# Kernel optimization log

Hardware: AMD Instinct MI355X
Metric: run time of the kernel (lower is better)

## Reference

```python
import jax, jax.numpy as jnp
import numpy as np

VOCAB = 50257
H = 1024
T = 4096


def setup_inputs() -> dict:
    key = jax.random.key(0)
    ks = jax.random.split(key, 6)
    scale = 1.0 / np.sqrt(H)  # matches torch LSTM uniform(-1/sqrt(H), 1/sqrt(H)) scale
    return {
        "tokens": jax.random.randint(ks[0], (T,), 0, VOCAB),
        "emb": jax.random.normal(ks[1], (VOCAB, H), dtype=jnp.float32) * 0.02,
        "w_ih": jax.random.uniform(ks[2], (4 * H, H), jnp.float32, -scale, scale),
        "w_hh": jax.random.uniform(ks[3], (4 * H, H), jnp.float32, -scale, scale),
        "b_ih": jax.random.uniform(ks[4], (4 * H,), jnp.float32, -scale, scale),
        "b_hh": jax.random.uniform(ks[5], (4 * H,), jnp.float32, -scale, scale),
    }


def _lstm(x, w_ih, w_hh, b_ih, b_hh):
    # x: [T, H]. Precompute input-side gate projections for all timesteps.
    gx = x @ w_ih.T + (b_ih + b_hh)  # [T, 4H]

    def step(carry, g_t):
        h, c = carry  # [H], [H]
        gates = g_t + h @ w_hh.T  # [4H]
        i, f, g, o = jnp.split(gates, 4)  # torch gate order: input, forget, cell, output
        i = jax.nn.sigmoid(i)
        f = jax.nn.sigmoid(f)
        g = jnp.tanh(g)
        o = jax.nn.sigmoid(o)
        c = f * c + i * g
        h = o * jnp.tanh(c)
        return (h, c), h

    h0 = jnp.zeros((H,), x.dtype)
    c0 = jnp.zeros((H,), x.dtype)
    (h_f, c_f), hs = jax.lax.scan(step, (h0, c0), gx)
    return hs, h_f, c_f  # hs: [T, H]


def reference(tokens, emb, w_ih, w_hh, b_ih, b_hh):
    x = emb[tokens]  # [T, H] embedding lookup
    hs, h_f, c_f = _lstm(x, w_ih, w_hh, b_ih, b_hh)
    output = hs[None, :, :]          # [1, T, H]  (batch_first, batch=1)
    h_n = h_f[None, None, :]         # [1, 1, H]
    c_n = c_f[None, None, :]         # [1, 1, H]
    return (output, (h_n, c_n))
```

## Files before the change

### kernel.cpp

```cpp
#include <hip/hip_runtime.h>
#include <hip/hip_bf16.h>

#define HD   1024
#define GD   4096
#define TT   4096
#define NWG  256
#define MBS  16

#define BM 128
#define BN 128
#define BK 16
#define LDP 132

__global__ __launch_bounds__(256, 2) void gemm_gx(
    const int* __restrict__ tokens,
    const float* __restrict__ emb,
    const float* __restrict__ Wih,
    const float* __restrict__ bih,
    const float* __restrict__ bhh,
    float* __restrict__ gxout)
{
    __shared__ float As[BK][LDP];
    __shared__ float Bs[BK][LDP];
    const int tid = threadIdx.x;
    const int m0 = blockIdx.x * BM;
    const int n0 = blockIdx.y * BN;
    const int tx = tid & 15;
    const int ty = tid >> 4;

    const int quad = tid & 3;
    const int r0   = tid >> 2;
    const int tok0 = tokens[m0 + r0];
    const int tok1 = tokens[m0 + r0 + 64];

    float acc[8][8] = {};

    for (int kt = 0; kt < HD; kt += BK) {
        float4 av0 = *reinterpret_cast<const float4*>(
            &emb[(size_t)tok0 * HD + kt + quad * 4]);
        float4 bv0 = *reinterpret_cast<const float4*>(
            &Wih[(size_t)(n0 + r0) * HD + kt + quad * 4]);
        float4 av1 = *reinterpret_cast<const float4*>(
            &emb[(size_t)tok1 * HD + kt + quad * 4]);
        float4 bv1 = *reinterpret_cast<const float4*>(
            &Wih[(size_t)(n0 + r0 + 64) * HD + kt + quad * 4]);
        As[quad * 4 + 0][r0] = av0.x;
        As[quad * 4 + 1][r0] = av0.y;
        As[quad * 4 + 2][r0] = av0.z;
        As[quad * 4 + 3][r0] = av0.w;
        Bs[quad * 4 + 0][r0] = bv0.x;
        Bs[quad * 4 + 1][r0] = bv0.y;
        Bs[quad * 4 + 2][r0] = bv0.z;
        Bs[quad * 4 + 3][r0] = bv0.w;
        As[quad * 4 + 0][r0 + 64] = av1.x;
        As[quad * 4 + 1][r0 + 64] = av1.y;
        As[quad * 4 + 2][r0 + 64] = av1.z;
        As[quad * 4 + 3][r0 + 64] = av1.w;
        Bs[quad * 4 + 0][r0 + 64] = bv1.x;
        Bs[quad * 4 + 1][r0 + 64] = bv1.y;
        Bs[quad * 4 + 2][r0 + 64] = bv1.z;
        Bs[quad * 4 + 3][r0 + 64] = bv1.w;
        __syncthreads();
#pragma unroll
        for (int k = 0; k < BK; ++k) {
            float4 a0 = *reinterpret_cast<const float4*>(&As[k][ty * 8]);
            float4 a1 = *reinterpret_cast<const float4*>(&As[k][ty * 8 + 4]);
            float4 b0 = *reinterpret_cast<const float4*>(&Bs[k][tx * 8]);
            float4 b1 = *reinterpret_cast<const float4*>(&Bs[k][tx * 8 + 4]);
            float a[8] = {a0.x, a0.y, a0.z, a0.w, a1.x, a1.y, a1.z, a1.w};
            float b[8] = {b0.x, b0.y, b0.z, b0.w, b1.x, b1.y, b1.z, b1.w};
#pragma unroll
            for (int i = 0; i < 8; ++i)
#pragma unroll
                for (int j = 0; j < 8; ++j)
                    acc[i][j] += a[i] * b[j];
        }
        __syncthreads();
    }

    float bias[8];
#pragma unroll
    for (int j = 0; j < 8; ++j) {
        int n = n0 + tx * 8 + j;
        bias[j] = bih[n] + bhh[n];
    }
#pragma unroll
    for (int i = 0; i < 8; ++i) {
        size_t o = (size_t)(m0 + ty * 8 + i) * GD + n0 + tx * 8;
        float4 s0 = {acc[i][0] + bias[0], acc[i][1] + bias[1],
                     acc[i][2] + bias[2], acc[i][3] + bias[3]};
        float4 s1 = {acc[i][4] + bias[4], acc[i][5] + bias[5],
                     acc[i][6] + bias[6], acc[i][7] + bias[7]};
        *reinterpret_cast<float4*>(&gxout[o]) = s0;
        *reinterpret_cast<float4*>(&gxout[o + 4]) = s1;
    }
}

__device__ __forceinline__ float sigmoid_(float x) {
    return 1.f / (1.f + __expf(-x));
}
__device__ __forceinline__ float tanh_(float x) {
    return __builtin_fmaf(2.f, 1.f / (1.f + __expf(-2.f * x)), -1.f);
}
__device__ __forceinline__ float bcast_(float v, int l) {
    return __uint_as_float(__builtin_amdgcn_readlane(__float_as_uint(v), l));
}
__device__ __forceinline__ void lds_barrier_() {
    asm volatile("s_waitcnt lgkmcnt(0)" ::: "memory");
    __builtin_amdgcn_s_barrier();
}

__global__ __launch_bounds__(256, 1) void lstm_scan(
    const float* __restrict__ gx,
    const float* __restrict__ whh,
    float* __restrict__ out,
    unsigned long long* __restrict__ hbuf)
{
    const int tid   = threadIdx.x;
    const int b     = blockIdx.x;
    const int lane  = tid & 63;
    const int wv    = tid >> 6;
    const int chunk = lane & 15;
    const int gate  = lane >> 4;
    const int j     = b * 4 + wv;
    const int R     = gate * HD + j;

    float w[64];
    {
        const float* wrow = whh + (size_t)R * HD;
#pragma unroll
        for (int q = 0; q < 16; ++q) {
            float4 v = *reinterpret_cast<const float4*>(&wrow[chunk * 4 + q * 64]);
            w[q * 4 + 0] = v.x; w[q * 4 + 1] = v.y;
            w[q * 4 + 2] = v.z; w[q * 4 + 3] = v.w;
        }
    }

    __shared__ float h_lds[2][HD];
#pragma unroll
    for (int q = 0; q < 4; ++q) h_lds[0][tid * 4 + q] = 0.f;
    lds_barrier_();

    float c_reg = 0.f;
    float gx_cur = gx[R];

    unsigned long long* const mp0 = hbuf + (size_t)(tid * 4) * MBS;
    unsigned long long* const mp1 = hbuf + (size_t)(HD + tid * 4) * MBS;

    for (int s = 1; s <= TT; ++s) {
        const int cb = (s - 1) & 1;
        const int nb = s & 1;

        float gx_nxt = 0.f;
        if (s < TT) gx_nxt = gx[(size_t)s * GD + R];

        float A0 = (chunk == 0) ? gx_cur : 0.f;
        float A1 = 0.f, A2 = 0.f, A3 = 0.f;
        {
            const float* hb = h_lds[cb];
#pragma unroll
            for (int q = 0; q < 4; ++q) {
                float4 h0 = *reinterpret_cast<const float4*>(&hb[chunk * 4 + (4 * q + 0) * 64]);
                float4 h1 = *reinterpret_cast<const float4*>(&hb[chunk * 4 + (4 * q + 1) * 64]);
                float4 h2 = *reinterpret_cast<const float4*>(&hb[chunk * 4 + (4 * q + 2) * 64]);
                float4 h3 = *reinterpret_cast<const float4*>(&hb[chunk * 4 + (4 * q + 3) * 64]);
                A0 = __builtin_fmaf(w[(4 * q + 0) * 4 + 0], h0.x, A0);
                A0 = __builtin_fmaf(w[(4 * q + 0) * 4 + 1], h0.y, A0);
                A0 = __builtin_fmaf(w[(4 * q + 0) * 4 + 2], h0.z, A0);
                A0 = __builtin_fmaf(w[(4 * q + 0) * 4 + 3], h0.w, A0);
                A1 = __builtin_fmaf(w[(4 * q + 1) * 4 + 0], h1.x, A1);
                A1 = __builtin_fmaf(w[(4 * q + 1) * 4 + 1], h1.y, A1);
                A1 = __builtin_fmaf(w[(4 * q + 1) * 4 + 2], h1.z, A1);
                A1 = __builtin_fmaf(w[(4 * q + 1) * 4 + 3], h1.w, A1);
                A2 = __builtin_fmaf(w[(4 * q + 2) * 4 + 0], h2.x, A2);
                A2 = __builtin_fmaf(w[(4 * q + 2) * 4 + 1], h2.y, A2);
                A2 = __builtin_fmaf(w[(4 * q + 2) * 4 + 2], h2.z, A2);
                A2 = __builtin_fmaf(w[(4 * q + 2) * 4 + 3], h2.w, A2);
                A3 = __builtin_fmaf(w[(4 * q + 3) * 4 + 0], h3.x, A3);
                A3 = __builtin_fmaf(w[(4 * q + 3) * 4 + 1], h3.y, A3);
                A3 = __builtin_fmaf(w[(4 * q + 3) * 4 + 2], h3.z, A3);
                A3 = __builtin_fmaf(w[(4 * q + 3) * 4 + 3], h3.w, A3);
            }
        }
        float acc = (A0 + A1) + (A2 + A3);
        acc += __shfl_xor(acc, 1, 64);
        acc += __shfl_xor(acc, 2, 64);
        acc += __shfl_xor(acc, 4, 64);
        acc += __shfl_xor(acc, 8, 64);
        float si = bcast_(acc, 0);
        float sf = bcast_(acc, 16);
        float sg = bcast_(acc, 32);
        float so = bcast_(acc, 48);

        float ii = sigmoid_(si);
        float ff = sigmoid_(sf);
        float gg = tanh_(sg);
        float oo = sigmoid_(so);
        c_reg = __builtin_fmaf(ff, c_reg, ii * gg);
        float hh = oo * tanh_(c_reg);

        if (s < TT) {
            if (lane == 0) {
                unsigned long long pkt =
                    ((unsigned long long)(unsigned)s << 32) | __float_as_uint(hh);
                __hip_atomic_store(&hbuf[(size_t)(nb * HD + j) * MBS], pkt,
                                   __ATOMIC_RELAXED, __HIP_MEMORY_SCOPE_AGENT);
            }
            gx_cur = gx_nxt;

            if (tid != b) {
                unsigned long long* src = nb ? mp1 : mp0;
                const unsigned long long tg = (unsigned long long)(unsigned)s;
                unsigned long long v0, v1, v2, v3;
                int r = 0;
                for (;;) {
                    v0 = __hip_atomic_load(&src[0 * MBS], __ATOMIC_RELAXED,
                                           __HIP_MEMORY_SCOPE_AGENT);
                    v1 = __hip_atomic_load(&src[1 * MBS], __ATOMIC_RELAXED,
                                           __HIP_MEMORY_SCOPE_AGENT);
                    v2 = __hip_atomic_load(&src[2 * MBS], __ATOMIC_RELAXED,
                                           __HIP_MEMORY_SCOPE_AGENT);
                    v3 = __hip_atomic_load(&src[3 * MBS], __ATOMIC_RELAXED,
                                           __HIP_MEMORY_SCOPE_AGENT);
                    unsigned long long bad = ((v0 >> 32) ^ tg) | ((v1 >> 32) ^ tg) |
                                             ((v2 >> 32) ^ tg) | ((v3 >> 32) ^ tg);
                    if (!bad) break;
                    ++r;
                    if (r > (1 << 17)) break;
                    if (r >= 2) __builtin_amdgcn_s_sleep(1);
                }
                float4 hv;
                hv.x = __uint_as_float((unsigned int)v0);
                hv.y = __uint_as_float((unsigned int)v1);
                hv.z = __uint_as_float((unsigned int)v2);
                hv.w = __uint_as_float((unsigned int)v3);
                *reinterpret_cast<float4*>(&h_lds[nb][tid * 4]) = hv;
            }
            if (lane == 0) {
                h_lds[nb][j] = hh;
                out[(size_t)(s - 1) * HD + j] = hh;
            }
            lds_barrier_();
        } else {
            if (lane == 0) {
                out[(size_t)(s - 1) * HD + j] = hh;
                out[(size_t)TT * HD + j] = hh;
                out[(size_t)TT * HD + HD + j] = c_reg;
            }
        }
    }
}

extern "C" void kernel_launch(void* const* d_in, const int* in_sizes, int n_in,
                              void* d_out, int out_size, void* d_ws, size_t ws_size,
                              hipStream_t stream) {
    const int*   tokens = (const int*)d_in[0];
    const float* emb    = (const float*)d_in[1];
    const float* w_ih   = (const float*)d_in[2];
    const float* w_hh   = (const float*)d_in[3];
    const float* b_ih   = (const float*)d_in[4];
    const float* b_hh   = (const float*)d_in[5];
    float* out = (float*)d_out;

    char* ws = (char*)d_ws;
    const size_t HBUF_BYTES = (size_t)2 * HD * MBS * 8;
    unsigned long long* hbuf = (unsigned long long*)ws;
    float* gx = (float*)(ws + HBUF_BYTES);

    hipMemsetAsync(hbuf, 0, HBUF_BYTES, stream);
    gemm_gx<<<dim3(TT / BM, GD / BN), 256, 0, stream>>>(tokens, emb, w_ih,
                                                        b_ih, b_hh, gx);
    lstm_scan<<<NWG, 256, 0, stream>>>(gx, w_hh, out, hbuf);
}
```

Baseline: 16.22 ms.

## Pack h-exchange mailboxes densely and poll with vectorized sc1 loads

The per-step hidden-state mailbox stops padding each 64-bit packet to its own 128-byte slot and packs them contiguously, so each thread polls its four packets with two 16-byte global loads (inline asm with sc1) in place of four separate atomic loads. The thread-to-slot mapping is rotated by block index so different workgroups poll different cache lines first, and spinning continues longer before sleeping. The aim is fewer memory transactions per poll and lower cross-workgroup synchronization latency per timestep. The trade-off is more false sharing on the written lines, and the visibility of the inline-asm loads now depends on the sc1 cache-policy bits.

```diff
diff --git a/kernel.cpp b/kernel.cpp
--- a/kernel.cpp
+++ b/kernel.cpp
@@ -5,7 +5,6 @@
 #define GD   4096
 #define TT   4096
 #define NWG  256
-#define MBS  16
 
 #define BM 128
 #define BN 128
@@ -110,6 +109,8 @@
     __builtin_amdgcn_s_barrier();
 }
 
+using u32x4 = __attribute__((ext_vector_type(4))) unsigned int;
+
 __global__ __launch_bounds__(256, 1) void lstm_scan(
     const float* __restrict__ gx,
     const float* __restrict__ whh,
@@ -144,8 +145,9 @@
     float c_reg = 0.f;
     float gx_cur = gx[R];
 
-    unsigned long long* const mp0 = hbuf + (size_t)(tid * 4) * MBS;
-    unsigned long long* const mp1 = hbuf + (size_t)(HD + tid * 4) * MBS;
+    const int tp = (tid + b) & 255;
+    unsigned long long* const pb0 = hbuf + (size_t)tp * 4;
+    unsigned long long* const pb1 = hbuf + HD + (size_t)tp * 4;
 
     for (int s = 1; s <= TT; ++s) {
         const int cb = (s - 1) & 1;
@@ -203,38 +205,37 @@
             if (lane == 0) {
                 unsigned long long pkt =
                     ((unsigned long long)(unsigned)s << 32) | __float_as_uint(hh);
-                __hip_atomic_store(&hbuf[(size_t)(nb * HD + j) * MBS], pkt,
+                __hip_atomic_store(&hbuf[(size_t)nb * HD + j], pkt,
                                    __ATOMIC_RELAXED, __HIP_MEMORY_SCOPE_AGENT);
             }
             gx_cur = gx_nxt;
 
-            if (tid != b) {
-                unsigned long long* src = nb ? mp1 : mp0;
-                const unsigned long long tg = (unsigned long long)(unsigned)s;
-                unsigned long long v0, v1, v2, v3;
+            if (tid != 0) {
+                const unsigned int us = (unsigned int)s;
+                unsigned long long* src = nb ? pb1 : pb0;
+                u32x4 q0, q1;
                 int r = 0;
                 for (;;) {
-                    v0 = __hip_atomic_load(&src[0 * MBS], __ATOMIC_RELAXED,
-                                           __HIP_MEMORY_SCOPE_AGENT);
-                    v1 = __hip_atomic_load(&src[1 * MBS], __ATOMIC_RELAXED,
-                                           __HIP_MEMORY_SCOPE_AGENT);
-                    v2 = __hip_atomic_load(&src[2 * MBS], __ATOMIC_RELAXED,
-                                           __HIP_MEMORY_SCOPE_AGENT);
-                    v3 = __hip_atomic_load(&src[3 * MBS], __ATOMIC_RELAXED,
-                                           __HIP_MEMORY_SCOPE_AGENT);
-                    unsigned long long bad = ((v0 >> 32) ^ tg) | ((v1 >> 32) ^ tg) |
-                                             ((v2 >> 32) ^ tg) | ((v3 >> 32) ^ tg);
-                    if (!bad) break;
+                    asm volatile(
+                        "global_load_dwordx4 %0, %2, off sc1\n\t"
+                        "global_load_dwordx4 %1, %2, off offset:16 sc1\n\t"
+                        "s_waitcnt vmcnt(0)"
+                        : "=v"(q0), "=v"(q1)
+                        : "v"(src)
+                        : "memory");
+                    bool ok = (q0.y == us) & (q0.w == us) &
+                              (q1.y == us) & (q1.w == us);
+                    if (ok) break;
                     ++r;
                     if (r > (1 << 17)) break;
-                    if (r >= 2) __builtin_amdgcn_s_sleep(1);
+                    if (r >= 6) __builtin_amdgcn_s_sleep(1);
                 }
                 float4 hv;
-                hv.x = __uint_as_float((unsigned int)v0);
-                hv.y = __uint_as_float((unsigned int)v1);
-                hv.z = __uint_as_float((unsigned int)v2);
-                hv.w = __uint_as_float((unsigned int)v3);
-                *reinterpret_cast<float4*>(&h_lds[nb][tid * 4]) = hv;
+                hv.x = __uint_as_float(q0.x);
+                hv.y = __uint_as_float(q0.z);
+                hv.z = __uint_as_float(q1.x);
+                hv.w = __uint_as_float(q1.z);
+                *reinterpret_cast<float4*>(&h_lds[nb][tp * 4]) = hv;
             }
             if (lane == 0) {
                 h_lds[nb][j] = hh;
@@ -263,9 +264,9 @@
     float* out = (float*)d_out;
 
     char* ws = (char*)d_ws;
-    const size_t HBUF_BYTES = (size_t)2 * HD * MBS * 8;
+    const size_t HBUF_BYTES = (size_t)2 * HD * 8;
     unsigned long long* hbuf = (unsigned long long*)ws;
-    float* gx = (float*)(ws + HBUF_BYTES);
+    float* gx = (float*)(ws + 65536);
 
     hipMemsetAsync(hbuf, 0, HBUF_BYTES, stream);
     gemm_gx<<<dim3(TT / BM, GD / BN), 256, 0, stream>>>(tokens, emb, w_ih,
```

New measurement: 18.78 ms. 1.16x slower.
